# Optimization experiments

Hardware: AMD Instinct MI355X
Metric: run time of the kernel (lower is better)

The kernel has to match this reference:

```python
import jax, jax.numpy as jnp
import numpy as np

B, T, C = 2, 2048, 1024
H = 16
HD = C // H

def setup_inputs() -> dict:
    key = jax.random.key(0)
    ks = jax.random.split(key, 5)
    scale = 0.02
    return {
        "x": jax.random.normal(ks[0], (B, T, C), jnp.float32),
        "w_attn": jax.random.normal(ks[1], (3 * C, C), jnp.float32) * scale,
        "b_attn": jnp.zeros((3 * C,), jnp.float32),
        "w_proj": jax.random.normal(ks[2], (C, C), jnp.float32) * scale,
        "b_proj": jnp.zeros((C,), jnp.float32),
    }

def reference(x, w_attn, b_attn, w_proj, b_proj):
    Bx, Tx, Cx = x.shape
    # qkv projection (torch Linear: x @ W^T + b)
    qkv = x @ w_attn.T + b_attn                     # [B,T,3C]
    q, k, v = jnp.split(qkv, 3, axis=2)
    # [B,T,C] -> [B,H,T,hd]
    def to_heads(t):
        return t.reshape(Bx, Tx, H, HD).transpose(0, 2, 1, 3)
    q, k, v = to_heads(q), to_heads(k), to_heads(v)
    scores = jnp.einsum('bhqd,bhkd->bhqk', q, k) / np.sqrt(HD).astype(jnp.float32)
    causal_mask = jnp.triu(jnp.ones((Tx, Tx), bool), k=1)   # True above diagonal
    scores = jnp.where(causal_mask, -jnp.inf, scores)
    attn = jax.nn.softmax(scores, axis=-1)
    y = jnp.einsum('bhqk,bhkd->bhqd', attn, v)      # [B,H,T,hd]
    y = y.transpose(0, 2, 1, 3).reshape(Bx, Tx, Cx)
    return y @ w_proj.T + b_proj
```

## Files before the change

kernel.cpp:

```cpp
#include <hip/hip_runtime.h>
#include <hip/hip_bf16.h>

using bf16 = __hip_bfloat16;

typedef __bf16 bf16x8 __attribute__((ext_vector_type(8)));
typedef __bf16 bf16x4v __attribute__((ext_vector_type(4)));
typedef float  float4v __attribute__((ext_vector_type(4)));
typedef unsigned short u16x8 __attribute__((ext_vector_type(8)));

#define MFMA16x16x32(a, b, c) __builtin_amdgcn_mfma_f32_16x16x32_bf16((a), (b), (c), 0, 0, 0)

#if __has_builtin(__builtin_amdgcn_exp2f)
#define EXP2F(x) __builtin_amdgcn_exp2f(x)
#else
#define EXP2F(x) exp2f(x)
#endif

#define T_SEQ 2048
#define NHEAD 16
#define CDIM  1024
#define HD3   3072

__device__ __forceinline__ void async_copy16(const void* g, void* l) {
    __builtin_amdgcn_global_load_lds(
        (__attribute__((address_space(1))) unsigned int*)g,
        (__attribute__((address_space(3))) unsigned int*)l,
        16, 0, 0);
}

__global__ __launch_bounds__(256) void convert_detect_kernel(
    const float* __restrict__ x, const float* __restrict__ wa,
    const float* __restrict__ wp,
    bf16* __restrict__ xb, bf16* __restrict__ wab, bf16* __restrict__ wpb,
    int* __restrict__ flag)
{
    __shared__ int red[256];
    const u16x8* xs8 = (const u16x8*)x;
    int cnt = 0;
    for (int i = threadIdx.x; i < 2048; i += 256) {
        const u16x8 v = xs8[i];
#pragma unroll
        for (int t = 0; t < 8; ++t) {
            const int e = (v[t] >> 7) & 0xFF;
            if (e == 0xFF || (e != 0 && e < 0x60)) cnt++;
        }
    }
    red[threadIdx.x] = cnt;
    __syncthreads();
    for (int s = 128; s > 0; s >>= 1) {
        if (threadIdx.x < s) red[threadIdx.x] += red[threadIdx.x + s];
        __syncthreads();
    }
    const int isf32 = (red[0] > 100) ? 1 : 0;
    if (blockIdx.x == 0 && threadIdx.x == 0) flag[0] = isf32;
    if (!isf32) return;

    const int gid    = blockIdx.x * 256 + threadIdx.x;
    const int stride = gridDim.x * 256;
    const float4v* x4  = (const float4v*)x;
    const float4v* wa4 = (const float4v*)wa;
    const float4v* wp4 = (const float4v*)wp;
    bf16x4v* xb4  = (bf16x4v*)xb;
    bf16x4v* wab4 = (bf16x4v*)wab;
    bf16x4v* wpb4 = (bf16x4v*)wpb;

    for (int i = gid; i < 1048576; i += stride) {
        const float4v v = x4[i];
        bf16x4v o;
#pragma unroll
        for (int t = 0; t < 4; ++t) o[t] = (__bf16)v[t];
        xb4[i] = o;
    }
    for (int i = gid; i < 786432; i += stride) {
        const float4v v = wa4[i];
        bf16x4v o;
#pragma unroll
        for (int t = 0; t < 4; ++t) o[t] = (__bf16)v[t];
        wab4[i] = o;
    }
    for (int i = gid; i < 262144; i += stride) {
        const float4v v = wp4[i];
        bf16x4v o;
#pragma unroll
        for (int t = 0; t < 4; ++t) o[t] = (__bf16)v[t];
        wpb4[i] = o;
    }
}

template<int JF>
__global__ __launch_bounds__(256) void gemm_nt_lds_t(
    const void* __restrict__ Araw, const bf16* __restrict__ Aconv,
    const void* __restrict__ Braw, const bf16* __restrict__ Bconv,
    const void* __restrict__ biasraw, void* __restrict__ Cv,
    int M, int N, int K, const int* __restrict__ flag, int is_final,
    int scale_q, int swz)
{
    const bool f32 = (flag[0] != 0);
    const bf16* A = f32 ? Aconv : (const bf16*)Araw;
    const bf16* B = f32 ? Bconv : (const bf16*)Braw;

    __shared__ bf16 As[128 * 64];
    __shared__ bf16 Bs[JF * 32 * 64];

    const int tid  = threadIdx.x;
    const int lane = tid & 63;
    const int wave = tid >> 6;
    const int wm = wave & 1, wn = wave >> 1;
    const int c = lane & 15, g = lane >> 4;

    int bx = blockIdx.x, by = blockIdx.y;
    if (swz) {
        const int nwg = gridDim.x * gridDim.y;
        const int lin = by * gridDim.x + bx;
        const int nl  = (lin & 7) * (nwg >> 3) + (lin >> 3);
        bx = nl % gridDim.x;
        by = nl / gridDim.x;
    }
    const int bm = bx * 128;
    const int bn = by * (JF * 32);

    const int srow = tid >> 3;
    const int slc  = ((tid & 7) ^ (srow & 7)) * 8;
    const bf16* gA = A + (size_t)(bm + srow) * K + slc;
    const bf16* gB = B + (size_t)(bn + srow) * K + slc;

    float4v acc[4][JF] = {};

    for (int k0 = 0; k0 < K; k0 += 64) {
        __syncthreads();
#pragma unroll
        for (int q = 0; q < 4; ++q)
            async_copy16(gA + k0 + (size_t)(q * 32) * K, As + q * 2048 + tid * 8);
#pragma unroll
        for (int q = 0; q < JF; ++q)
            async_copy16(gB + k0 + (size_t)(q * 32) * K, Bs + q * 2048 + tid * 8);
        __syncthreads();

#pragma unroll
        for (int kk = 0; kk < 2; ++kk) {
            bf16x8 af[4], bfr[JF];
#pragma unroll
            for (int i = 0; i < 4; ++i)
                af[i]  = *(const bf16x8*)&As[(wm * 64 + i * 16 + c) * 64 +
                                             (((kk * 4 + g) ^ (c & 7)) * 8)];
#pragma unroll
            for (int j = 0; j < JF; ++j)
                bfr[j] = *(const bf16x8*)&Bs[(wn * (JF * 16) + j * 16 + c) * 64 +
                                             (((kk * 4 + g) ^ (c & 7)) * 8)];
#pragma unroll
            for (int i = 0; i < 4; ++i)
#pragma unroll
                for (int j = 0; j < JF; ++j)
                    acc[i][j] = MFMA16x16x32(af[i], bfr[j], acc[i][j]);
        }
    }

    const bool f32o = is_final && f32;
    bf16*  Cb = (bf16*)Cv;
    float* Cf = (float*)Cv;

#pragma unroll
    for (int i = 0; i < 4; ++i) {
        const int row = bm + wm * 64 + i * 16 + g * 4;
#pragma unroll
        for (int j = 0; j < JF; ++j) {
            const int col = bn + wn * (JF * 16) + j * 16 + c;
            const float bv = f32 ? ((const float*)biasraw)[col]
                                 : __bfloat162float(((const bf16*)biasraw)[col]);
            const float sc = (scale_q && col < 1024) ? 0.18033688f : 1.0f;
            if (f32o) {
#pragma unroll
                for (int t = 0; t < 4; ++t)
                    Cf[(size_t)(row + t) * N + col] = (acc[i][j][t] + bv) * sc;
            } else {
#pragma unroll
                for (int t = 0; t < 4; ++t)
                    Cb[(size_t)(row + t) * N + col] =
                        __float2bfloat16((acc[i][j][t] + bv) * sc);
            }
        }
    }
}

__global__ __launch_bounds__(512) void attn_mfma(
    const bf16* __restrict__ qkv, bf16* __restrict__ y)
{
    __shared__ __bf16 Ks[2][128 * 64];
    __shared__ __bf16 Vt[2][64 * 128];

    const int tid  = threadIdx.x;
    const int lane = tid & 63;
    const int w    = tid >> 6;
    const int c    = lane & 15;
    const int g    = lane >> 4;

    const int i    = blockIdx.x;
    const int role = i >> 8;
    const int bhl  = i & 7;
    const int t5   = (i & 255) >> 3;
    const int j    = t5 >> 2;
    const int bh   = ((t5 & 3) << 3) | bhl;
    const int qblk = role ? j : (15 - j);
    const int bb   = bh >> 4;
    const int h    = bh & 15;
    const size_t base = (size_t)bb * T_SEQ * HD3 + (size_t)h * 64;

    const bool kstage = (tid < 256);
    const int st   = tid & 255;
    const int krow = st >> 3;
    const int klc  = ((st & 7) ^ (krow & 7)) * 8;
    const int kq   = st & 31;
    const int dgv  = st >> 5;
    const int vchunk = (kq >> 3) * 4 + (kq & 3);
    const int vlow   = ((kq >> 2) & 1) * 4;

    const bf16* kgbase = qkv + base + 1024;
    const bf16* vgbase = qkv + base + 2048;

    bf16x8 ones;
#pragma unroll
    for (int ii = 0; ii < 8; ++ii) ones[ii] = (__bf16)1.0f;

    const int q0 = qblk * 128;
    const int qw = q0 + w * 16;

    bf16x8 qf[2];
#pragma unroll
    for (int kf2 = 0; kf2 < 2; ++kf2)
        qf[kf2] = *(const bf16x8*)(qkv + base
            + (size_t)(qw + c) * HD3 + kf2 * 32 + g * 8);

    float4v o[4] = {};
    float4v ol = {};

    if (kstage) {
#pragma unroll
        for (int q = 0; q < 4; ++q)
            async_copy16(kgbase + (size_t)(q * 32 + krow) * HD3 + klc,
                         &Ks[0][q * 2048 + st * 8]);
    } else {
        bf16x8 vr[4];
#pragma unroll
        for (int r = 0; r < 4; ++r)
            vr[r] = *(const bf16x8*)(vgbase + (size_t)(kq * 4 + r) * HD3 + dgv * 8);
#pragma unroll
        for (int jj = 0; jj < 8; ++jj) {
            const int d = dgv * 8 + jj;
            bf16x4v pk;
#pragma unroll
            for (int r = 0; r < 4; ++r) pk[r] = vr[r][jj];
            *(bf16x4v*)&Vt[0][d * 128 + ((vchunk ^ (d & 7)) << 3) + vlow] = pk;
        }
    }
    __syncthreads();

    int b = 0;
    for (int kt = 0; kt <= q0; kt += 128, b ^= 1) {
        const bool more = (kt + 128 <= q0);
        bf16x8 vr[4];
        if (more) {
            if (kstage) {
#pragma unroll
                for (int q = 0; q < 4; ++q)
                    async_copy16(kgbase + (size_t)(kt + 128 + q * 32 + krow) * HD3 + klc,
                                 &Ks[b ^ 1][q * 2048 + st * 8]);
            } else {
#pragma unroll
                for (int r = 0; r < 4; ++r)
                    vr[r] = *(const bf16x8*)(vgbase + (size_t)(kt + 128 + kq * 4 + r) * HD3 + dgv * 8);
            }
        }

#pragma unroll
        for (int hf = 0; hf < 2; ++hf) {
            if (kt + hf * 64 > qw + 15) continue;

            float4v sacc[4] = {};
            __builtin_amdgcn_s_setprio(1);
#pragma unroll
            for (int jb = 0; jb < 4; ++jb) {
                const int key = hf * 64 + jb * 16 + c;
                bf16x8 a0 = *(const bf16x8*)&Ks[b][key * 64 + ((g ^ (c & 7)) * 8)];
                bf16x8 a1 = *(const bf16x8*)&Ks[b][key * 64 + (((4 + g) ^ (c & 7)) * 8)];
                sacc[jb] = MFMA16x16x32(a0, qf[0], sacc[jb]);
                sacc[jb] = MFMA16x16x32(a1, qf[1], sacc[jb]);
            }
            __builtin_amdgcn_s_setprio(0);

            bf16x8 pf[2];
            {
                if (kt + hf * 64 + 63 > qw) {
                    const int query = qw + c;
#pragma unroll
                    for (int jb = 0; jb < 4; ++jb) {
                        const int kb = kt + hf * 64 + jb * 16 + g * 4;
#pragma unroll
                        for (int t = 0; t < 4; ++t)
                            if (kb + t > query) sacc[jb][t] = -1e30f;
                    }
                }
#pragma unroll
                for (int jb = 0; jb < 4; ++jb)
#pragma unroll
                    for (int t = 0; t < 4; ++t)
                        sacc[jb][t] = EXP2F(sacc[jb][t]);
#pragma unroll
                for (int lkf = 0; lkf < 2; ++lkf) {
                    bf16x8 pk;
#pragma unroll
                    for (int jj = 0; jj < 8; ++jj)
                        pk[jj] = (__bf16)sacc[lkf * 2 + (jj >> 2)][jj & 3];
                    pf[lkf] = pk;
                }
            }

            __builtin_amdgcn_s_setprio(1);
#pragma unroll
            for (int lkf = 0; lkf < 2; ++lkf) {
                const int kf = hf * 2 + lkf;
                ol = MFMA16x16x32(ones, pf[lkf], ol);
#pragma unroll
                for (int dn = 0; dn < 4; ++dn) {
                    const int d = dn * 16 + c;
                    bf16x8 vf = *(const bf16x8*)
                        &Vt[b][d * 128 + (((kf * 4 + g) ^ (d & 7)) << 3)];
                    o[dn] = MFMA16x16x32(vf, pf[lkf], o[dn]);
                }
            }
            __builtin_amdgcn_s_setprio(0);
        }

        if (more && !kstage) {
#pragma unroll
            for (int jj = 0; jj < 8; ++jj) {
                const int d = dgv * 8 + jj;
                bf16x4v pk;
#pragma unroll
                for (int r = 0; r < 4; ++r) pk[r] = vr[r][jj];
                *(bf16x4v*)&Vt[b ^ 1][d * 128 + ((vchunk ^ (d & 7)) << 3) + vlow] = pk;
            }
        }
        __syncthreads();
    }

    {
        const float linv = 1.f / ol.x;
        const int q = qw + c;
        const size_t yb = ((size_t)bb * T_SEQ + q) * CDIM + h * 64;
#pragma unroll
        for (int dn = 0; dn < 4; ++dn) {
            bf16x4v ov;
#pragma unroll
            for (int t = 0; t < 4; ++t)
                ov[t] = (__bf16)(o[dn][t] * linv);
            *(bf16x4v*)&y[yb + dn * 16 + g * 4] = ov;
        }
    }
}

extern "C" void kernel_launch(void* const* d_in, const int* in_sizes, int n_in,
                              void* d_out, int out_size, void* d_ws, size_t ws_size,
                              hipStream_t stream)
{
    const int M = 4096;
    char* ws = (char*)d_ws;

    int*  flag = (int*)ws;
    bf16* xb   = (bf16*)(ws + 256);
    bf16* wab  = (bf16*)(ws + 8388864);
    bf16* wpb  = (bf16*)(ws + 14680320);
    bf16* qkv  = (bf16*)(ws + 16777472);
    bf16* yb   = (bf16*)(ws + 41943296);

    convert_detect_kernel<<<512, 256, 0, stream>>>(
        (const float*)d_in[0], (const float*)d_in[1], (const float*)d_in[3],
        xb, wab, wpb, flag);

    {
        dim3 grid(M / 128, 3072 / 64);
        gemm_nt_lds_t<2><<<grid, 256, 0, stream>>>(d_in[0], xb, d_in[1], wab,
                                                   d_in[2], qkv, M, 3072, 1024,
                                                   flag, 0, 1, 1);
    }
    {
        attn_mfma<<<512, 512, 0, stream>>>(qkv, yb);
    }
    {
        dim3 grid(M / 128, 1024 / 64);
        gemm_nt_lds_t<2><<<grid, 256, 0, stream>>>(yb, yb, d_in[3], wpb,
                                                   d_in[4], d_out, M, 1024, 1024,
                                                   flag, 1, 0, 1);
    }
    (void)in_sizes; (void)n_in; (void)out_size; (void)ws_size;
}
```

Before: 182.0 us.

## Triple-buffer GEMM LDS tiles with async prefetch two stages ahead

```diff
diff --git a/kernel.cpp b/kernel.cpp
--- a/kernel.cpp
+++ b/kernel.cpp
@@ -95,12 +95,13 @@
     int M, int N, int K, const int* __restrict__ flag, int is_final,
     int scale_q, int swz)
 {
+    static_assert(JF == 2, "vmcnt(6) literal assumes 4 A + 2 B loads/thread");
     const bool f32 = (flag[0] != 0);
     const bf16* A = f32 ? Aconv : (const bf16*)Araw;
     const bf16* B = f32 ? Bconv : (const bf16*)Braw;
 
-    __shared__ bf16 As[128 * 64];
-    __shared__ bf16 Bs[JF * 32 * 64];
+    __shared__ bf16 As[3][128 * 64];
+    __shared__ bf16 Bs[3][JF * 32 * 64];
 
     const int tid  = threadIdx.x;
     const int lane = tid & 63;
@@ -126,33 +127,52 @@
 
     float4v acc[4][JF] = {};
 
-    for (int k0 = 0; k0 < K; k0 += 64) {
-        __syncthreads();
+    const int nk = K >> 6;
+
+    auto stage = [&](int t, int buf) {
 #pragma unroll
         for (int q = 0; q < 4; ++q)
-            async_copy16(gA + k0 + (size_t)(q * 32) * K, As + q * 2048 + tid * 8);
+            async_copy16(gA + t * 64 + (size_t)(q * 32) * K,
+                         &As[buf][q * 2048 + tid * 8]);
 #pragma unroll
         for (int q = 0; q < JF; ++q)
-            async_copy16(gB + k0 + (size_t)(q * 32) * K, Bs + q * 2048 + tid * 8);
-        __syncthreads();
+            async_copy16(gB + t * 64 + (size_t)(q * 32) * K,
+                         &Bs[buf][q * 2048 + tid * 8]);
+    };
+
+    stage(0, 0);
+    stage(1, 1);
+    asm volatile("s_waitcnt vmcnt(6)" ::: "memory");
+    __builtin_amdgcn_s_barrier();
+
+    int b = 0;
+    for (int t = 0; t < nk; ++t) {
+        const bool deep = (t + 2 < nk);
+        if (deep) stage(t + 2, (b + 2 >= 3) ? b - 1 : b + 2);
 
 #pragma unroll
         for (int kk = 0; kk < 2; ++kk) {
             bf16x8 af[4], bfr[JF];
 #pragma unroll
             for (int i = 0; i < 4; ++i)
-                af[i]  = *(const bf16x8*)&As[(wm * 64 + i * 16 + c) * 64 +
-                                             (((kk * 4 + g) ^ (c & 7)) * 8)];
+                af[i]  = *(const bf16x8*)&As[b][(wm * 64 + i * 16 + c) * 64 +
+                                               (((kk * 4 + g) ^ (c & 7)) * 8)];
 #pragma unroll
             for (int j = 0; j < JF; ++j)
-                bfr[j] = *(const bf16x8*)&Bs[(wn * (JF * 16) + j * 16 + c) * 64 +
-                                             (((kk * 4 + g) ^ (c & 7)) * 8)];
+                bfr[j] = *(const bf16x8*)&Bs[b][(wn * (JF * 16) + j * 16 + c) * 64 +
+                                               (((kk * 4 + g) ^ (c & 7)) * 8)];
 #pragma unroll
             for (int i = 0; i < 4; ++i)
 #pragma unroll
                 for (int j = 0; j < JF; ++j)
                     acc[i][j] = MFMA16x16x32(af[i], bfr[j], acc[i][j]);
         }
+
+        if (deep) asm volatile("s_waitcnt vmcnt(6)" ::: "memory");
+        else      asm volatile("s_waitcnt vmcnt(0)" ::: "memory");
+        __builtin_amdgcn_s_barrier();
+
+        b = (b == 2) ? 0 : b + 1;
     }
 
     const bool f32o = is_final && f32;
```

Measured after the change: 191.5 us. +5.2%, slower.
